# Performance work log

Measured on AMD Instinct MI355X. Metric: run time of the kernel, lower is better.

## Reference

```python
import jax, jax.numpy as jnp
import numpy as np

N = 8192
F_IN = 128
F_OUT = 128
E = 262144
ALPHA = 0.2  # LeakyReLU negative slope
NEG_INF = -1e20


def setup_inputs() -> dict:
    key = jax.random.key(0)
    k_x, k_e, k_w, k_a = jax.random.split(key, 4)
    x = jax.random.normal(k_x, (N, F_IN), dtype=jnp.float32)
    edge_index = jax.random.randint(k_e, (2, E), 0, N, dtype=jnp.int64)
    # xavier_uniform with gain=1.414
    gain = 1.414
    bw = gain * np.sqrt(6.0 / (F_IN + F_OUT))
    W = jax.random.uniform(k_w, (F_IN, F_OUT), minval=-bw, maxval=bw, dtype=jnp.float32)
    ba = gain * np.sqrt(6.0 / (2 * F_OUT + 1))
    a = jax.random.uniform(k_a, (2 * F_OUT, 1), minval=-ba, maxval=ba, dtype=jnp.float32)
    bias = jnp.zeros((F_OUT,), dtype=jnp.float32)
    return {"x": x, "edge_index": edge_index, "W": W, "a": a, "bias": bias}


def reference(x, edge_index, W, a, bias):
    # dropout is identity in eval mode (training=False)
    h = x @ W  # [N, F_OUT]
    source, target = edge_index[0], edge_index[1]
    # cat([h[src], h[dst]]) @ a == h[src] @ a[:F] + h[dst] @ a[F:]
    a_src, a_dst = a[:F_OUT, 0], a[F_OUT:, 0]
    e = (h @ a_src)[source] + (h @ a_dst)[target]  # [E]
    e = jax.nn.leaky_relu(e, negative_slope=ALPHA)
    n = h.shape[0]
    attention = jnp.full((n, n), NEG_INF, dtype=h.dtype)
    attention = attention.at[source, target].set(e)
    attention = jax.nn.softmax(attention, axis=1)
    h_prime = attention @ h + bias
    return h_prime
```

## Files before the change

kernel.cpp:

```cpp
#include <hip/hip_runtime.h>

#define N_NODES 8192
#define F 128
#define NEDGE 262144
#define ALPHA 0.2f
#define SLOTS 128

static const size_t WS_CURSOR = 0;
static const size_t WS_MEANH  = 32768;
static const size_t WS_ZERO_BYTES = 33280;
static const size_t WS_CSR    = 33792;
static const size_t WS_H      = 4228096;
static const size_t WS_SVAL   = 8422400;
static const size_t WS_DVAL   = 8455168;

__global__ __launch_bounds__(256) void fused_kernel(const float* __restrict__ x,
                                                    const float* __restrict__ W,
                                                    const float* __restrict__ a,
                                                    const int* __restrict__ src,
                                                    const int* __restrict__ tgt,
                                                    float* __restrict__ h,
                                                    float* __restrict__ sval,
                                                    float* __restrict__ dval,
                                                    float* __restrict__ meanh,
                                                    int* __restrict__ cursor,
                                                    int* __restrict__ csr) {
  __shared__ float shW[32][128];
  __shared__ float shx[16][32];
  __shared__ float sred[16][128];
  int tid = threadIdx.x;

  if (blockIdx.x >= 512) {
    int k = (blockIdx.x - 512) * 256 + tid;
    int s = src[k];
    int t = tgt[k];
    int pos = atomicAdd(&cursor[s], 1);
    if (pos < SLOTS) csr[s * SLOTS + pos] = t;
    return;
  }

  int row0 = blockIdx.x * 16;
  int col  = tid & 127;
  int half = tid >> 7;
  float acc[8] = {0.f,0.f,0.f,0.f,0.f,0.f,0.f,0.f};
  for (int kk = 0; kk < 128; kk += 32) {
    #pragma unroll
    for (int i = 0; i < 16; ++i) {
      int idx = i * 256 + tid;
      shW[idx >> 7][idx & 127] = W[(kk + (idx >> 7)) * 128 + (idx & 127)];
    }
    #pragma unroll
    for (int i = 0; i < 2; ++i) {
      int idx = i * 256 + tid;
      shx[idx >> 5][idx & 31] = x[(row0 + (idx >> 5)) * 128 + kk + (idx & 31)];
    }
    __syncthreads();
    #pragma unroll
    for (int k = 0; k < 32; ++k) {
      float wv = shW[k][col];
      #pragma unroll
      for (int q = 0; q < 8; ++q)
        acc[q] += shx[half + 2 * q][k] * wv;
    }
    __syncthreads();
  }
  #pragma unroll
  for (int q = 0; q < 8; ++q)
    h[(row0 + half + 2 * q) * 128 + col] = acc[q];

  int wid  = tid >> 6;
  int lane = tid & 63;
  float as = a[col];
  float ad = a[128 + col];

  #pragma unroll
  for (int q = 0; q < 8; ++q) sred[half + 2 * q][col] = acc[q] * as;
  __syncthreads();
  #pragma unroll
  for (int r = 0; r < 4; ++r) {
    int rr = 4 * wid + r;
    float v = sred[rr][lane] + sred[rr][lane + 64];
    #pragma unroll
    for (int off = 32; off; off >>= 1) v += __shfl_xor(v, off);
    if (lane == 0) sval[row0 + rr] = v;
  }
  __syncthreads();

  #pragma unroll
  for (int q = 0; q < 8; ++q) sred[half + 2 * q][col] = acc[q] * ad;
  __syncthreads();
  #pragma unroll
  for (int r = 0; r < 4; ++r) {
    int rr = 4 * wid + r;
    float v = sred[rr][lane] + sred[rr][lane + 64];
    #pragma unroll
    for (int off = 32; off; off >>= 1) v += __shfl_xor(v, off);
    if (lane == 0) dval[row0 + rr] = v;
  }
  __syncthreads();

  float m = 0.f;
  #pragma unroll
  for (int q = 0; q < 8; ++q) m += acc[q];
  float* flat = &sred[0][0];
  flat[tid] = m;
  __syncthreads();
  if (tid < 128) atomicAdd(&meanh[tid], flat[tid] + flat[tid + 128]);
}

__global__ __launch_bounds__(256) void row_kernel(const float* __restrict__ h,
                                                  const float* __restrict__ sval,
                                                  const float* __restrict__ dval,
                                                  const int* __restrict__ cursor,
                                                  const int* __restrict__ csr,
                                                  const float* __restrict__ bias,
                                                  const float* __restrict__ meanh,
                                                  float* __restrict__ out) {
  int row  = blockIdx.x * 4 + (threadIdx.x >> 6);
  int lane = threadIdx.x & 63;
  int L = cursor[row];
  if (L > SLOTS) L = SLOTS;
  float2 b2 = ((const float2*)bias)[lane];

  if (L == 0) {
    float2 m2 = ((const float2*)meanh)[lane];
    float2 o;
    o.x = m2.x * (1.0f / N_NODES) + b2.x;
    o.y = m2.y * (1.0f / N_NODES) + b2.y;
    ((float2*)out)[row * 64 + lane] = o;
    return;
  }

  const int* rcsr = csr + row * SLOTS;
  float sr = sval[row];
  int t0 = (lane      < L) ? rcsr[lane]      : -1;
  int t1 = (lane + 64 < L) ? rcsr[lane + 64] : -1;
  float w0 = 0.f, w1 = 0.f;
  if (t0 >= 0) { float e = sr + dval[t0]; e = e > 0.f ? e : ALPHA * e; w0 = __expf(e); }
  if (t1 >= 0) { float e = sr + dval[t1]; e = e > 0.f ? e : ALPHA * e; w1 = __expf(e); }

  const float2* h2 = (const float2*)h;
  float2 acc = make_float2(0.f, 0.f);
  float z = 0.f;
  #pragma unroll 2
  for (int l = 0; l < L; ++l) {
    int   sel  = l & 63;
    int   tsrc = (l < 64) ? t0 : t1;
    float wsrc = (l < 64) ? w0 : w1;
    int   tl = __builtin_amdgcn_readlane(tsrc, sel);
    float wl = __int_as_float(__builtin_amdgcn_readlane(__float_as_int(wsrc), sel));
    bool mine_earlier = (t0 == tl && lane < l) || (t1 == tl && lane + 64 < l);
    float we = (__ballot(mine_earlier) == 0ULL) ? wl : 0.f;
    float2 hv = h2[tl * 64 + lane];
    z     += we;
    acc.x += we * hv.x;
    acc.y += we * hv.y;
  }
  float inv_z = 1.0f / z;
  float2 o;
  o.x = acc.x * inv_z + b2.x;
  o.y = acc.y * inv_z + b2.y;
  ((float2*)out)[row * 64 + lane] = o;
}

extern "C" void kernel_launch(void* const* d_in, const int* in_sizes, int n_in,
                              void* d_out, int out_size, void* d_ws, size_t ws_size,
                              hipStream_t stream) {
  const float* x    = (const float*)d_in[0];
  const int*   ei   = (const int*)d_in[1];
  const float* W    = (const float*)d_in[2];
  const float* a    = (const float*)d_in[3];
  const float* bias = (const float*)d_in[4];
  float* out = (float*)d_out;

  char* ws = (char*)d_ws;
  int*   cursor = (int*)(ws + WS_CURSOR);
  float* meanh  = (float*)(ws + WS_MEANH);
  int*   csr    = (int*)(ws + WS_CSR);
  float* h      = (float*)(ws + WS_H);
  float* sval   = (float*)(ws + WS_SVAL);
  float* dval   = (float*)(ws + WS_DVAL);

  const int* src = ei;
  const int* tgt = ei + NEDGE;

  hipMemsetAsync(ws, 0, WS_ZERO_BYTES, stream);
  fused_kernel<<<1536, 256, 0, stream>>>(x, W, a, src, tgt, h, sval, dval,
                                         meanh, cursor, csr);
  row_kernel<<<N_NODES / 4, 256, 0, stream>>>(h, sval, dval, cursor, csr,
                                              bias, meanh, out);
}
```

Before: 108.6 us.

## Split each row's edge list across two wavefronts and combine via shared memory

The row aggregation kernel now assigns two wavefronts per output row, each handling half of the row's neighbor list, and merges partial accumulators and normalizers through shared memory. The goal is to halve the serial gather loop length per wave and raise memory-level parallelism for the h row gathers. Deduplication across halves is handled by comparing against the first half's targets. It doubles the grid size and adds block-wide barriers and a shared-memory reduction.

```diff
diff --git a/kernel.cpp b/kernel.cpp
--- a/kernel.cpp
+++ b/kernel.cpp
@@ -116,51 +116,74 @@
                                                   const float* __restrict__ bias,
                                                   const float* __restrict__ meanh,
                                                   float* __restrict__ out) {
-  int row  = blockIdx.x * 4 + (threadIdx.x >> 6);
-  int lane = threadIdx.x & 63;
+  __shared__ int    shT[2][64];
+  __shared__ float2 shAcc[2][64];
+  __shared__ float  shZ[2];
+
+  int tid  = threadIdx.x;
+  int w    = tid >> 6;
+  int rib  = w >> 1;
+  int part = w & 1;
+  int lane = tid & 63;
+  int row  = blockIdx.x * 2 + rib;
+
   int L = cursor[row];
   if (L > SLOTS) L = SLOTS;
-  float2 b2 = ((const float2*)bias)[lane];
-
-  if (L == 0) {
-    float2 m2 = ((const float2*)meanh)[lane];
-    float2 o;
-    o.x = m2.x * (1.0f / N_NODES) + b2.x;
-    o.y = m2.y * (1.0f / N_NODES) + b2.y;
-    ((float2*)out)[row * 64 + lane] = o;
-    return;
-  }
+  int LA  = (L + 1) >> 1;
+  int myN = part ? (L - LA) : LA;
+  int base = part ? LA : 0;
 
   const int* rcsr = csr + row * SLOTS;
   float sr = sval[row];
-  int t0 = (lane      < L) ? rcsr[lane]      : -1;
-  int t1 = (lane + 64 < L) ? rcsr[lane + 64] : -1;
-  float w0 = 0.f, w1 = 0.f;
-  if (t0 >= 0) { float e = sr + dval[t0]; e = e > 0.f ? e : ALPHA * e; w0 = __expf(e); }
-  if (t1 >= 0) { float e = sr + dval[t1]; e = e > 0.f ? e : ALPHA * e; w1 = __expf(e); }
+
+  int   t   = (lane < myN) ? rcsr[base + lane] : -1;
+  float wgt = 0.f;
+  if (t >= 0) {
+    float e = sr + dval[t];
+    e = e > 0.f ? e : ALPHA * e;
+    wgt = __expf(e);
+  }
+
+  if (part == 0) shT[rib][lane] = t;
+  __syncthreads();
+  int pa = part ? shT[rib][lane] : -1;
 
   const float2* h2 = (const float2*)h;
   float2 acc = make_float2(0.f, 0.f);
   float z = 0.f;
   #pragma unroll 2
-  for (int l = 0; l < L; ++l) {
-    int   sel  = l & 63;
-    int   tsrc = (l < 64) ? t0 : t1;
-    float wsrc = (l < 64) ? w0 : w1;
-    int   tl = __builtin_amdgcn_readlane(tsrc, sel);
-    float wl = __int_as_float(__builtin_amdgcn_readlane(__float_as_int(wsrc), sel));
-    bool mine_earlier = (t0 == tl && lane < l) || (t1 == tl && lane + 64 < l);
-    float we = (__ballot(mine_earlier) == 0ULL) ? wl : 0.f;
+  for (int l = 0; l < myN; ++l) {
+    int   tl = __builtin_amdgcn_readlane(t, l);
+    float wl = __int_as_float(__builtin_amdgcn_readlane(__float_as_int(wgt), l));
+    bool dup = (pa == tl) || (t == tl && lane < l);
+    float we = (__ballot(dup) == 0ULL) ? wl : 0.f;
     float2 hv = h2[tl * 64 + lane];
     z     += we;
     acc.x += we * hv.x;
     acc.y += we * hv.y;
   }
-  float inv_z = 1.0f / z;
-  float2 o;
-  o.x = acc.x * inv_z + b2.x;
-  o.y = acc.y * inv_z + b2.y;
-  ((float2*)out)[row * 64 + lane] = o;
+
+  if (part == 1) {
+    shAcc[rib][lane] = acc;
+    if (lane == 0) shZ[rib] = z;
+  }
+  __syncthreads();
+
+  if (part == 0) {
+    float2 b2 = ((const float2*)bias)[lane];
+    float2 o;
+    if (L == 0) {
+      float2 m2 = ((const float2*)meanh)[lane];
+      o.x = m2.x * (1.0f / N_NODES) + b2.x;
+      o.y = m2.y * (1.0f / N_NODES) + b2.y;
+    } else {
+      float2 ab = shAcc[rib][lane];
+      float inv_z = 1.0f / (z + shZ[rib]);
+      o.x = (acc.x + ab.x) * inv_z + b2.x;
+      o.y = (acc.y + ab.y) * inv_z + b2.y;
+    }
+    ((float2*)out)[row * 64 + lane] = o;
+  }
 }
 
 extern "C" void kernel_launch(void* const* d_in, const int* in_sizes, int n_in,
@@ -187,6 +210,6 @@
   hipMemsetAsync(ws, 0, WS_ZERO_BYTES, stream);
   fused_kernel<<<1536, 256, 0, stream>>>(x, W, a, src, tgt, h, sval, dval,
                                          meanh, cursor, csr);
-  row_kernel<<<N_NODES / 4, 256, 0, stream>>>(h, sval, dval, cursor, csr,
+  row_kernel<<<N_NODES / 2, 256, 0, stream>>>(h, sval, dval, cursor, csr,
                                               bias, meanh, out);
 }
```

Result: no change. 109.4 us (+0.8%).
